# Performance work log

Measured on AMD Instinct MI355X. Metric: run time of the kernel, lower is better.

## Reference

```python
import jax, jax.numpy as jnp
import numpy as np

B, T, N, PRED, DM = 16, 512, 128, 256, 32
L = T + PRED  # 768; conv windows 12 then 4: 768 -> 64 -> 16
EPS = 1e-5


def _conv1d(x, w, b, stride):
    # x: [B, C, L'], w: [C, C, k], kernel_size == stride, VALID (matches torch Conv1d)
    out = jax.lax.conv_general_dilated(x, w, (stride,), 'VALID',
                                       dimension_numbers=('NCH', 'OIH', 'NCH'))
    return out + b[None, :, None]


def _conv2d(x, w, b, pad):
    out = jax.lax.conv_general_dilated(x, w, (1, 1), [(pad, pad), (pad, pad)],
                                       dimension_numbers=('NCHW', 'OIHW', 'NCHW'))
    return out + b[None, :, None, None]


def _bn1d(x, g, b):
    # BatchNorm1d, training-mode batch statistics over (batch, length) per channel
    mu = x.mean((0, 2), keepdims=True)
    var = ((x - mu) ** 2).mean((0, 2), keepdims=True)
    return (x - mu) * jax.lax.rsqrt(var + EPS) * g[None, :, None] + b[None, :, None]


def _cubic_spline(y, size):
    # Natural cubic spline through values y: [B, Lk, C] at knots t = linspace(0,1,Lk),
    # evaluated at linspace(0,1,size). Natural BC: second derivative M=0 at endpoints.
    Bb, Lk, C = y.shape
    h = 1.0 / (Lk - 1)
    # tridiagonal system for interior second derivatives (uniform knots):
    # M[i-1] + 4 M[i] + M[i+1] = 6 * (y[i+1] - 2 y[i] + y[i-1]) / h^2
    m = Lk - 2
    rhs = (y[:, 2:, :] - 2.0 * y[:, 1:-1, :] + y[:, :-2, :]) * (6.0 / (h * h))  # [B,m,C]
    A = 4.0 * jnp.eye(m, dtype=y.dtype) + jnp.eye(m, k=1, dtype=y.dtype) + jnp.eye(m, k=-1, dtype=y.dtype)
    Mi = jnp.linalg.solve(A, rhs.transpose(1, 0, 2).reshape(m, Bb * C))  # [m, B*C]
    Mi = Mi.reshape(m, Bb, C).transpose(1, 0, 2)
    M = jnp.pad(Mi, ((0, 0), (1, 1), (0, 0)))  # [B, Lk, C], M[0]=M[-1]=0
    q = jnp.linspace(0.0, 1.0, size).astype(y.dtype)
    idx = jnp.clip(jnp.floor(q * (Lk - 1)).astype(jnp.int32), 0, Lk - 2)  # [size]
    s = (q - idx.astype(y.dtype) * h)[None, :, None]  # offset within interval
    u = h - s
    yi, yi1 = y[:, idx, :], y[:, idx + 1, :]
    M0, M1 = M[:, idx, :], M[:, idx + 1, :]
    hh6 = h * h / 6.0
    return ((M0 * u ** 3 + M1 * s ** 3) / (6.0 * h)
            + (yi - M0 * hh6) * (u / h)
            + (yi1 - M1 * hh6) * (s / h))  # [B, size, C]


def _forward(batch_x, le_w, le_b, c1_w, c1_b, bn1_g, bn1_b, c2_w, c2_b, bn2_g, bn2_b,
             i1_w0, i1_b0, i1_w1, i1_b1, i2_w0, i2_b0, i2_w1, i2_b1, ld_w, ld_b):
    # instance norm over time
    means = batch_x.mean(1, keepdims=True)
    xc = batch_x - means
    stdev = jnp.sqrt(xc.var(axis=1, keepdims=True) + EPS)
    xn = xc / stdev                               # [B, T, N]
    x = xn.transpose(0, 2, 1)                     # [B, N, T]
    x = jnp.einsum('bnt,lt->bnl', x, le_w) + le_b  # length_encoder -> [B, N, L]
    # multi-scale downsampling conv + spline back up to L
    scales = []
    t = x
    for win, cw, cb, g, bb in ((12, c1_w, c1_b, bn1_g, bn1_b), (4, c2_w, c2_b, bn2_g, bn2_b)):
        t = jax.nn.elu(_bn1d(_conv1d(t, cw, cb, win), g, bb))      # [B, N, L//...]
        scales.append(_cubic_spline(t.transpose(0, 2, 1), L).transpose(0, 2, 1))  # [B, N, L]
    a = jnp.stack([x] + scales, axis=1).transpose(0, 1, 3, 2)  # [B, 3, L, N]
    # Inception block 1 (num_kernels=2: 1x1 and 3x3, averaged), Dropout(eval)=id, GELU(exact)
    h1 = 0.5 * (_conv2d(a, i1_w0, i1_b0, 0) + _conv2d(a, i1_w1, i1_b1, 1))  # [B, DM, L, N]
    h1 = jax.nn.gelu(h1, approximate=False)
    # Inception block 2 -> 1 channel
    h2 = 0.5 * (_conv2d(h1, i2_w0, i2_b0, 0) + _conv2d(h1, i2_w1, i2_b1, 1))  # [B, 1, L, N]
    co = x + h2[:, 0].transpose(0, 2, 1)          # residual, [B, N, L]
    f = jnp.einsum('bnl,pl->bnp', co, ld_w) + ld_b  # length_decoder -> [B, N, PRED]
    f = f.transpose(0, 2, 1)                      # [B, PRED, N]
    return f * stdev[:, 0, :][:, None, :] + means[:, 0, :][:, None, :]


def setup_inputs():
    key = jax.random.key(0)
    ks = jax.random.split(key, 20)
    def w(i, shape, scale=0.02):
        return scale * jax.random.normal(ks[i], shape, jnp.float32)
    return dict(
        batch_x=jax.random.normal(ks[0], (B, T, N), jnp.float32),
        batch_x_mark=jax.random.normal(ks[1], (B, T, 4), jnp.float32),
        dec_inp=jax.random.normal(ks[2], (B, PRED, N), jnp.float32),
        batch_y_mark=jax.random.normal(ks[3], (B, PRED, 4), jnp.float32),
        le_w=w(4, (L, T)), le_b=w(5, (L,)),
        c1_w=w(6, (N, N, 12)), c1_b=w(7, (N,)),
        bn1_g=jnp.ones((N,), jnp.float32), bn1_b=jnp.zeros((N,), jnp.float32),
        c2_w=w(8, (N, N, 4)), c2_b=w(9, (N,)),
        bn2_g=jnp.ones((N,), jnp.float32), bn2_b=jnp.zeros((N,), jnp.float32),
        i1_w0=w(10, (DM, 3, 1, 1), 0.1), i1_b0=jnp.zeros((DM,), jnp.float32),
        i1_w1=w(11, (DM, 3, 3, 3), 0.1), i1_b1=jnp.zeros((DM,), jnp.float32),
        i2_w0=w(12, (1, DM, 1, 1), 0.1), i2_b0=jnp.zeros((1,), jnp.float32),
        i2_w1=w(13, (1, DM, 3, 3), 0.1), i2_b1=jnp.zeros((1,), jnp.float32),
        ld_w=w(14, (PRED, L)), ld_b=w(15, (PRED,)),
    )


def reference(batch_x, batch_x_mark, dec_inp, batch_y_mark, le_w, le_b,
              c1_w, c1_b, bn1_g, bn1_b, c2_w, c2_b, bn2_g, bn2_b,
              i1_w0, i1_b0, i1_w1, i1_b1, i2_w0, i2_b0, i2_w1, i2_b1, ld_w, ld_b):
    # batch_x_mark / dec_inp / batch_y_mark are accepted but unused (as in the torch forward)
    return _forward(batch_x, le_w, le_b, c1_w, c1_b, bn1_g, bn1_b, c2_w, c2_b, bn2_g, bn2_b,
                    i1_w0, i1_b0, i1_w1, i1_b1, i2_w0, i2_b0, i2_w1, i2_b1, ld_w, ld_b)
```

## Files before the change

kernel.cpp:

```cpp
#include <hip/hip_runtime.h>
#include <hip/hip_bf16.h>
#include <math.h>

#define BB 16
#define TT 512
#define NN 128
#define PREDN 256
#define DMC 32
#define LL 768
constexpr float EPSF = 1e-5f;
using bf16 = __hip_bfloat16;
using frag_ab = __attribute__((ext_vector_type(8))) short;
using frag_cd = __attribute__((ext_vector_type(4))) float;

__device__ __forceinline__ unsigned pbf2(float a, float b){
  union { bf16 h; unsigned short u; } x, y;
  x.h = __float2bfloat16(a); y.h = __float2bfloat16(b);
  return (unsigned)x.u | ((unsigned)y.u << 16);
}

__device__ __forceinline__ unsigned short bf16b(float v){
  union { bf16 h; unsigned short u; } x;
  x.h = __float2bfloat16(v);
  return x.u;
}

__device__ __forceinline__ float gelu_fast(float s){
  float s2v = s*s;
  float e = exp2f(s*fmaf(s2v, 0.10294396f, 2.30211806f));
  return s*e*__builtin_amdgcn_rcpf(e + 1.f);
}

__global__ void k_pre(const float* __restrict__ bx, const float* __restrict__ v0,
                      const float* __restrict__ v1, const float* __restrict__ w1c,
                      const float* __restrict__ w2c, const float* __restrict__ w0s1,
                      const float* __restrict__ w1s1, const float* __restrict__ b0s1,
                      const float* __restrict__ b1s1, const float* __restrict__ lew,
                      const float* __restrict__ ldw,
                      float* __restrict__ muv, float* __restrict__ sdv,
                      unsigned short* __restrict__ xbf,
                      float* __restrict__ wT1, float* __restrict__ wT2,
                      uint4* __restrict__ bwpk, uint4* __restrict__ awpk,
                      float* __restrict__ bsum, unsigned* __restrict__ lewbf,
                      unsigned* __restrict__ ldwbf){
  __shared__ float sr[32][16], s2r[32][16], bmu[16], brs[16];
  __shared__ float ts[32][33];
  int blk = blockIdx.x;
  int tid = threadIdx.x;
  if(blk < 128){
    int b = blk >> 3, n0 = (blk & 7)*16;
    int c4 = (tid & 3)*4;
    int ch = tid >> 2;
    const float* p = bx + ((size_t)b*TT + ch*16)*NN + n0 + c4;
    float4 s = make_float4(0.f,0.f,0.f,0.f), s2 = make_float4(0.f,0.f,0.f,0.f);
    for(int t=0;t<16;t++){
      float4 v = *(const float4*)(p + (size_t)t*NN);
      s.x += v.x; s.y += v.y; s.z += v.z; s.w += v.w;
      s2.x += v.x*v.x; s2.y += v.y*v.y; s2.z += v.z*v.z; s2.w += v.w*v.w;
    }
    *(float4*)&sr[ch][c4] = s;
    *(float4*)&s2r[ch][c4] = s2;
    __syncthreads();
    if(tid < 16){
      float ss = 0.f, ss2 = 0.f;
      #pragma unroll 8
      for(int k2=0;k2<32;k2++){ ss += sr[k2][tid]; ss2 += s2r[k2][tid]; }
      float m = ss*(1.f/512.f);
      float var = fmaxf(ss2*(1.f/512.f) - m*m, 0.f);
      float sd = sqrtf(var + EPSF);
      muv[b*NN + n0 + tid] = m;
      sdv[b*NN + n0 + tid] = sd;
      bmu[tid] = m; brs[tid] = 1.f/sd;
    }
    __syncthreads();
    for(int i=tid; i<2048; i+=128){
      int t = i >> 2, g4 = (i & 3)*4;
      const float* q = bx + ((size_t)b*TT + t)*NN + n0 + g4;
      float4 v = *(const float4*)q;
      unsigned lo = pbf2((v.x - bmu[g4  ])*brs[g4  ], (v.y - bmu[g4+1])*brs[g4+1]);
      unsigned hi = pbf2((v.z - bmu[g4+2])*brs[g4+2], (v.w - bmu[g4+3])*brs[g4+3]);
      *(uint2*)&xbf[((size_t)b*TT + t)*NN + n0 + g4] = make_uint2(lo, hi);
    }
  } else if(blk < 320){
    int tt = blk - 128;
    int kt = tt % 48, ot = tt / 48;
    int k0 = kt*32, o0 = ot*32;
    for(int i=tid;i<1024;i+=128){ int r=i>>5, c=i&31; ts[r][c] = w1c[(size_t)(o0+r)*1536 + k0+c]; }
    __syncthreads();
    for(int i=tid;i<1024;i+=128){ int kr=i>>5, oc=i&31; wT1[(size_t)(k0+kr)*NN + o0+oc] = ts[oc][kr]; }
  } else if(blk < 384){
    int tt = blk - 320;
    int kt = tt % 16, ot = tt / 16;
    int k0 = kt*32, o0 = ot*32;
    for(int i=tid;i<1024;i+=128){ int r=i>>5, c=i&31; ts[r][c] = w2c[(size_t)(o0+r)*512 + k0+c]; }
    __syncthreads();
    for(int i=tid;i<1024;i+=128){ int kr=i>>5, oc=i&31; wT2[(size_t)(k0+kr)*NN + o0+oc] = ts[oc][kr]; }
  } else if(blk == 384){
    int i = tid;
    {
      int c = i >> 2, kq = i & 3;
      float w8[8];
      #pragma unroll
      for(int j=0;j<8;j++){
        int k = kq*8+j; float w = 0.f;
        if(k < 27){
          int ci = k/9, r9 = k - ci*9, dy = r9/3, dx = r9 - dy*3;
          w = 0.5f*w1s1[((c*3+ci)*3+dy)*3+dx];
          if(dy==1 && dx==1) w += 0.5f*w0s1[c*3+ci];
        }
        w8[j] = w;
      }
      bwpk[i] = make_uint4(pbf2(w8[0],w8[1]), pbf2(w8[2],w8[3]),
                           pbf2(w8[4],w8[5]), pbf2(w8[6],w8[7]));
    }
    if(i < 36){
      int tap = i >> 2, qq = i & 3, c8 = qq*8;
      float w8[8];
      #pragma unroll
      for(int j=0;j<8;j++){
        int c = c8 + j;
        w8[j] = 0.5f*v1[c*9 + tap] + ((tap==4) ? 0.5f*v0[c] : 0.f);
      }
      awpk[i] = make_uint4(pbf2(w8[0],w8[1]), pbf2(w8[2],w8[3]),
                           pbf2(w8[4],w8[5]), pbf2(w8[6],w8[7]));
    }
    if(i < 32) bsum[i] = 0.5f*(b0s1[i] + b1s1[i]);
  } else if(blk < 513){
    int o = blk - 385;
    for(int i=tid; i<1536; i+=128){
      int l = o*6 + i/256, tp = i%256;
      lewbf[(size_t)l*256 + tp] = pbf2(lew[(size_t)l*TT + 2*tp], lew[(size_t)l*TT + 2*tp + 1]);
    }
  } else {
    int o = blk - 513;
    for(int i=tid; i<1536; i+=128){
      int p = o*4 + i/384, tp = i%384;
      ldwbf[(size_t)p*384 + tp] = pbf2(ldw[(size_t)p*LL + 2*tp], ldw[(size_t)p*LL + 2*tp + 1]);
    }
  }
}

__global__ __launch_bounds__(256) void k_gemm1(const unsigned short* __restrict__ xbf,
    const unsigned* __restrict__ lewbf, const float* __restrict__ leb,
    float* __restrict__ x, float* __restrict__ a0){
  __shared__ unsigned Asu[64*20];
  __shared__ unsigned Bsu[64*20];
  int tid = threadIdx.x;
  int row0 = blockIdx.x*64, l0 = blockIdx.y*64;
  int b = row0 >> 7, n0 = row0 & 127;
  int lane = tid & 63, wv = tid >> 6;
  frag_cd acc[4] = {};
  int an = tid & 63, akq = (tid >> 6)*8;
  int btk = tid & 15, blc = tid >> 4;
  unsigned ra[4], rbq[4];
  #pragma unroll
  for(int u=0;u<4;u++){
    unsigned lo = xbf[((size_t)b*TT + akq + 2*u)*NN + n0 + an];
    unsigned hi = xbf[((size_t)b*TT + akq + 2*u + 1)*NN + n0 + an];
    ra[u] = lo | (hi << 16);
    rbq[u] = lewbf[(size_t)(l0 + blc + 16*u)*256 + btk];
  }
  int fr = wv*16 + (lane & 15);
  int fq = (lane >> 4)*4;
  for(int k0=0;k0<TT;k0+=32){
    *(uint4*)&Asu[an*20 + (akq>>1)] = make_uint4(ra[0], ra[1], ra[2], ra[3]);
    #pragma unroll
    for(int p=0;p<4;p++) Bsu[(blc + 16*p)*20 + btk] = rbq[p];
    __syncthreads();
    if(k0 + 32 < TT){
      #pragma unroll
      for(int u=0;u<4;u++){
        unsigned lo = xbf[((size_t)b*TT + k0 + 32 + akq + 2*u)*NN + n0 + an];
        unsigned hi = xbf[((size_t)b*TT + k0 + 32 + akq + 2*u + 1)*NN + n0 + an];
        ra[u] = lo | (hi << 16);
        rbq[u] = lewbf[(size_t)(l0 + blc + 16*u)*256 + ((k0 + 32) >> 1) + btk];
      }
    }
    frag_ab af = *(const frag_ab*)&Asu[fr*20 + fq];
    #pragma unroll
    for(int nt=0;nt<4;nt++){
      frag_ab bf = *(const frag_ab*)&Bsu[(nt*16 + (lane & 15))*20 + fq];
      acc[nt] = __builtin_amdgcn_mfma_f32_16x16x32_bf16(af, bf, acc[nt], 0, 0, 0);
    }
    __syncthreads();
  }
  int col = lane & 15, quad = lane >> 4;
  #pragma unroll
  for(int nt=0;nt<4;nt++){
    int l = l0 + nt*16 + col;
    float lb = leb[l];
    #pragma unroll
    for(int r=0;r<4;r++){
      int m = wv*16 + quad*4 + r;
      x[(size_t)(row0 + m)*LL + l] = acc[nt][r] + lb;
    }
    float4 st;
    st.x = acc[nt][0] + lb;
    st.y = acc[nt][1] + lb;
    st.z = acc[nt][2] + lb;
    st.w = acc[nt][3] + lb;
    *(float4*)&a0[((size_t)b*LL + l)*NN + n0 + wv*16 + quad*4] = st;
  }
}

__global__ __launch_bounds__(512) void k_conv1(const float* __restrict__ x, const float* __restrict__ wT,
                                               const float* __restrict__ bias, float* __restrict__ t1){
  __shared__ alignas(16) float xs[NN*48];
  int jt = blockIdx.x, b = blockIdx.y;
  int tid = threadIdx.x;
  int o = tid & 127, jj = tid >> 7;
  for(int i=tid;i<NN*48;i+=512){
    int ci = i/48, kk = i%48;
    xs[i] = x[((size_t)b*NN + ci)*LL + jt*48 + kk];
  }
  __syncthreads();
  float a0 = 0.f, a1 = 0.f, a2 = 0.f, a3 = 0.f;
  for(int ci=0;ci<NN;ci++){
    const float* xc = xs + ci*48 + jj*12;
    const float* wc = wT + (size_t)(ci*12)*NN + o;
    #pragma unroll
    for(int kk=0;kk<12;kk+=4){
      a0 = fmaf(xc[kk+0], wc[(size_t)(kk+0)*NN], a0);
      a1 = fmaf(xc[kk+1], wc[(size_t)(kk+1)*NN], a1);
      a2 = fmaf(xc[kk+2], wc[(size_t)(kk+2)*NN], a2);
      a3 = fmaf(xc[kk+3], wc[(size_t)(kk+3)*NN], a3);
    }
  }
  int j = jt*4 + jj;
  t1[((size_t)b*NN + o)*64 + j] = (a0 + a1) + (a2 + a3) + bias[o];
}

__global__ void k_bnstats(const float* __restrict__ t, const float* __restrict__ g, const float* __restrict__ bb,
                          int Bcnt, int Jcnt, float* __restrict__ scale, float* __restrict__ shift){
  int o = blockIdx.x;
  int tot = Bcnt*Jcnt;
  float s = 0.f, s2 = 0.f;
  for(int i=threadIdx.x; i<tot; i+=blockDim.x){
    int b = i / Jcnt, j = i % Jcnt;
    float v = t[((size_t)b*NN + o)*Jcnt + j];
    s += v; s2 += v*v;
  }
  __shared__ float rs[256], rs2[256];
  rs[threadIdx.x] = s; rs2[threadIdx.x] = s2;
  __syncthreads();
  for(int st=128; st>0; st>>=1){
    if(threadIdx.x < st){ rs[threadIdx.x] += rs[threadIdx.x+st]; rs2[threadIdx.x] += rs2[threadIdx.x+st]; }
    __syncthreads();
  }
  if(threadIdx.x == 0){
    float mu = rs[0]/tot;
    float var = fmaxf(rs2[0]/tot - mu*mu, 0.f);
    float sc = g[o] * rsqrtf(var + EPSF);
    scale[o] = sc; shift[o] = bb[o] - mu*sc;
  }
}

template<int LK>
__global__ __launch_bounds__(256) void k_bnspl(const float* __restrict__ t, const float* __restrict__ scale,
    const float* __restrict__ shift, float* __restrict__ tt, float* __restrict__ M){
  constexpr int m = LK-2;
  __shared__ float yt[LK][NN+1];
  __shared__ float cp[m];
  __shared__ float dp[m][NN];
  int b = blockIdx.x, tid = threadIdx.x;
  for(int i=tid; i<LK*NN; i+=256){
    int o = i / LK, j = i - o*LK;
    float v = t[((size_t)b*NN + o)*LK + j]*scale[o] + shift[o];
    v = v > 0.f ? v : (expf(v) - 1.f);
    yt[j][o] = v;
  }
  if(tid == 0){
    float cv = 0.25f; cp[0] = cv;
    for(int i=1;i<m;i++){ cv = 1.f/(4.f - cv); cp[i] = cv; }
  }
  __syncthreads();
  for(int i=tid; i<LK*NN; i+=256){
    int j = i >> 7, o = i & 127;
    tt[((size_t)b*LK + j)*NN + o] = yt[j][o];
  }
  if(tid < NN){
    int c = tid;
    const float Kc = 6.f*(LK-1)*(LK-1);
    float y0 = yt[0][c], y1 = yt[1][c];
    float dprev = 0.f;
    for(int i=0;i<m;i++){
      float y2 = yt[i+2][c];
      float r = (y2 - 2.f*y1 + y0)*Kc;
      float d = (i == 0) ? r*0.25f : (r - dprev)*cp[i];
      dp[i][c] = d; dprev = d;
      y0 = y1; y1 = y2;
    }
    float* Mb = M + (size_t)b*LK*NN + c;
    float xv = dp[m-1][c];
    Mb[(size_t)m*NN] = xv;
    for(int i=m-2;i>=0;i--){
      xv = dp[i][c] - cp[i]*xv;
      Mb[(size_t)(i+1)*NN] = xv;
    }
    Mb[0] = 0.f;
    Mb[(size_t)(LK-1)*NN] = 0.f;
  }
}

__global__ __launch_bounds__(512) void k_conv2(const float* __restrict__ tt, const float* __restrict__ wT,
                                               const float* __restrict__ bias, float* __restrict__ t2){
  __shared__ alignas(16) float ts[16*NN];
  int jt = blockIdx.x, b = blockIdx.y;
  int tid = threadIdx.x;
  int o = tid & 127, jj = tid >> 7;
  for(int i=tid;i<16*NN;i+=512)
    ts[i] = tt[((size_t)b*64 + jt*16)*NN + i];
  __syncthreads();
  float a0 = 0.f, a1 = 0.f, a2 = 0.f, a3 = 0.f;
  for(int ci=0;ci<NN;ci++){
    const float* wc = wT + (size_t)(ci*4)*NN + o;
    const float* tc2 = ts + (jj*4)*NN + ci;
    a0 = fmaf(tc2[0*NN], wc[0*NN], a0);
    a1 = fmaf(tc2[1*NN], wc[1*NN], a1);
    a2 = fmaf(tc2[2*NN], wc[2*NN], a2);
    a3 = fmaf(tc2[3*NN], wc[3*NN], a3);
  }
  int j = jt*4 + jj;
  t2[((size_t)b*NN + o)*16 + j] = (a0 + a1) + (a2 + a3) + bias[o];
}

template<int LK>
__device__ __forceinline__ void spline_pair(const float* __restrict__ y, const float* __restrict__ M,
    int l, int b, int c0, bool ok0, bool ok1, float& v0, float& v1){
  const float hh = 1.f/(LK-1);
  float q = (float)l * (1.f/(LL-1));
  int idx = (int)floorf(q*(LK-1));
  if(idx > LK-2) idx = LK-2;
  float s = q - idx*hh;
  float u = hh - s;
  const float hh6 = hh*hh/6.f;
  const float i6h = 1.f/(6.f*hh);
  const float ih = 1.f/hh;
  float cu = u*u*u, cs = s*s*s;
  float uh = u*ih, sh = s*ih;
  const float* yb = y + ((size_t)b*LK + idx)*NN + c0;
  const float* Mb = M + ((size_t)b*LK + idx)*NN + c0;
  v0 = 0.f; v1 = 0.f;
  if(ok0){
    float yi = yb[0], yi1 = yb[NN], M0 = Mb[0], M1 = Mb[NN];
    v0 = (M0*cu + M1*cs)*i6h + (yi - M0*hh6)*uh + (yi1 - M1*hh6)*sh;
  }
  if(ok1){
    float yi = yb[1], yi1 = yb[NN+1], M0 = Mb[1], M1 = Mb[NN+1];
    v1 = (M0*cu + M1*cs)*i6h + (yi - M0*hh6)*uh + (yi1 - M1*hh6)*sh;
  }
}

#define PBQ 1416
__global__ __launch_bounds__(256, 5) void k_h12(const float* __restrict__ a0,
    const float* __restrict__ y64, const float* __restrict__ M64,
    const float* __restrict__ y16, const float* __restrict__ M16,
    const uint4* __restrict__ bwpk, const uint4* __restrict__ awpk,
    const float* __restrict__ bsum, const float* __restrict__ vb0,
    const float* __restrict__ vb1, unsigned short* __restrict__ cobf){
  __shared__ alignas(16) unsigned short AsBf[3*12*36];
  __shared__ alignas(16) unsigned Au[4*PBQ];
  int tid = threadIdx.x;
  int l0 = blockIdx.x*8, n0 = blockIdx.y*32, b = blockIdx.z;
  int lane = tid & 63, wv = tid >> 6;
  int colB = lane & 15, qg = lane >> 4;

  for(int i=tid; i<648; i+=256){
    int ch = i/216, rem = i%216, yy = rem/18, xxp = rem%18;
    int xx = xxp*2;
    int gl = l0 + yy - 2, gn0 = n0 + xx - 2;
    bool okl = (gl >= 0 && gl < LL);
    bool ok0 = okl && ((unsigned)gn0 < (unsigned)NN);
    bool ok1 = okl && ((unsigned)(gn0+1) < (unsigned)NN);
    float v0 = 0.f, v1 = 0.f;
    if(ch == 0){
      if(ok0) v0 = a0[((size_t)b*LL + gl)*NN + gn0];
      if(ok1) v1 = a0[((size_t)b*LL + gl)*NN + gn0 + 1];
    } else if(okl){
      if(ch == 1) spline_pair<64>(y64, M64, gl, b, gn0, ok0, ok1, v0, v1);
      else        spline_pair<16>(y16, M16, gl, b, gn0, ok0, ok1, v0, v1);
    }
    *(unsigned*)&AsBf[i*2] = pbf2(v0, v1);
  }

  union U4 { uint4 q; frag_ab f; };
  U4 bw0, bw1;
  bw0.q = bwpk[colB*4 + qg];
  bw1.q = bwpk[(colB + 16)*4 + qg];
  float brA[4], brB[4];
  #pragma unroll
  for(int r=0;r<4;r++){ brA[r] = bsum[qg*4 + r]; brB[r] = bsum[16 + qg*4 + r]; }
  __syncthreads();

  {
    const unsigned* Uv = (const unsigned*)AsBf;
    if(tid < 176){
      if(tid < 170){
        int yy = tid/17, xp = tid - yy*17;
        unsigned g[3][3][2];
        #pragma unroll
        for(int ci=0;ci<3;ci++)
          #pragma unroll
          for(int dy=0;dy<3;dy++){
            int base = (ci*12 + yy + dy)*18 + xp;
            g[ci][dy][0] = Uv[base];
            g[ci][dy][1] = Uv[base+1];
          }
        int px0 = yy*34 + 2*xp;
        uint4 pq;
        pq.x = g[0][0][0];
        pq.y = (g[0][0][1]&0xffffu) | (g[0][1][0]<<16);
        pq.z = (g[0][1][0]>>16) | (g[0][1][1]<<16);
        pq.w = g[0][2][0];
        *(uint4*)&Au[0*PBQ + px0*4] = pq;
        pq.x = (g[0][2][1]&0xffffu) | (g[1][0][0]<<16);
        pq.y = (g[1][0][0]>>16) | (g[1][0][1]<<16);
        pq.z = g[1][1][0];
        pq.w = (g[1][1][1]&0xffffu) | (g[1][2][0]<<16);
        *(uint4*)&Au[1*PBQ + px0*4] = pq;
        pq.x = (g[1][2][0]>>16) | (g[1][2][1]<<16);
        pq.y = g[2][0][0];
        pq.z = (g[2][0][1]&0xffffu) | (g[2][1][0]<<16);
        pq.w = (g[2][1][0]>>16) | (g[2][1][1]<<16);
        *(uint4*)&Au[2*PBQ + px0*4] = pq;
        pq.x = g[2][2][0];
        pq.y = g[2][2][1]&0xffffu;
        pq.z = 0u; pq.w = 0u;
        *(uint4*)&Au[3*PBQ + px0*4] = pq;
        int px1 = px0 + 1;
        pq.x = (g[0][0][0]>>16) | (g[0][0][1]<<16);
        pq.y = (g[0][0][1]>>16) | (g[0][1][0]&0xffff0000u);
        pq.z = g[0][1][1];
        pq.w = (g[0][2][0]>>16) | (g[0][2][1]<<16);
        *(uint4*)&Au[0*PBQ + px1*4] = pq;
        pq.x = (g[0][2][1]>>16) | (g[1][0][0]&0xffff0000u);
        pq.y = g[1][0][1];
        pq.z = (g[1][1][0]>>16) | (g[1][1][1]<<16);
        pq.w = (g[1][1][1]>>16) | (g[1][2][0]&0xffff0000u);
        *(uint4*)&Au[1*PBQ + px1*4] = pq;
        pq.x = g[1][2][1];
        pq.y = (g[2][0][0]>>16) | (g[2][0][1]<<16);
        pq.z = (g[2][0][1]>>16) | (g[2][1][0]&0xffff0000u);
        pq.w = g[2][1][1];
        *(uint4*)&Au[2*PBQ + px1*4] = pq;
        pq.x = (g[2][2][0]>>16) | (g[2][2][1]<<16);
        pq.y = g[2][2][1]>>16;
        pq.z = 0u; pq.w = 0u;
        *(uint4*)&Au[3*PBQ + px1*4] = pq;
      } else {
        int px = 340 + (tid-170)*2;
        uint4 z = make_uint4(0u,0u,0u,0u);
        #pragma unroll
        for(int q=0;q<4;q++){
          *(uint4*)&Au[q*PBQ + px*4]     = z;
          *(uint4*)&Au[q*PBQ + (px+1)*4] = z;
        }
      }
    }
  }
  __syncthreads();

  unsigned short* h1h = (unsigned short*)Au;
  frag_cd zac = {0.f, 0.f, 0.f, 0.f};
  for(int t = wv; t < 22; t += 4){
    int px = t*16 + colB;
    U4 av;
    av.q = *(const uint4*)&Au[qg*PBQ + px*4];
    frag_cd d0 = __builtin_amdgcn_mfma_f32_16x16x32_bf16(bw0.f, av.f, zac, 0, 0, 0);
    frag_cd d1 = __builtin_amdgcn_mfma_f32_16x16x32_bf16(bw1.f, av.f, zac, 0, 0, 0);
    unsigned u0 = pbf2(gelu_fast(d0[0] + brA[0]), gelu_fast(d0[1] + brA[1]));
    unsigned u1 = pbf2(gelu_fast(d0[2] + brA[2]), gelu_fast(d0[3] + brA[3]));
    unsigned u2 = pbf2(gelu_fast(d1[0] + brB[0]), gelu_fast(d1[1] + brB[1]));
    unsigned u3 = pbf2(gelu_fast(d1[2] + brB[2]), gelu_fast(d1[3] + brB[3]));
    int lo = (qg >> 1)*PBQ + px*4 + (qg & 1)*2;
    *(uint2*)&Au[lo]           = make_uint2(u0, u1);
    *(uint2*)&Au[2*PBQ + lo]   = make_uint2(u2, u3);
  }
  __syncthreads();

  if(n0 == 0){
    for(int i=tid;i<10*32;i+=256){ int yy=i>>5, ch=i&31;
      h1h[((ch>>3)*PBQ + (yy*34)*4)*2 + (ch&7)] = 0; }
  }
  if(n0 == 96){
    for(int i=tid;i<10*32;i+=256){ int yy=i>>5, ch=i&31;
      h1h[((ch>>3)*PBQ + (yy*34+33)*4)*2 + (ch&7)] = 0; }
  }
  if(l0 == 0){
    for(int i=tid;i<34*32;i+=256){ int xx=i>>5, ch=i&31;
      h1h[((ch>>3)*PBQ + xx*4)*2 + (ch&7)] = 0; }
  }
  if(l0 == 760){
    for(int i=tid;i<34*32;i+=256){ int xx=i>>5, ch=i&31;
      h1h[((ch>>3)*PBQ + (9*34+xx)*4)*2 + (ch&7)] = 0; }
  }

  U4 aw[9];
  #pragma unroll
  for(int tap=0; tap<9; tap++) aw[tap].q = awpk[tap*4 + qg];
  float vbsum = vb0[0] + vb1[0];
  __syncthreads();

  frag_cd cacc[4] = {};
  int baseoff[4];
  #pragma unroll
  for(int tt=0; tt<4; tt++){
    int px = (wv*4 + tt)*16 + colB;
    int yy = px >> 5, xx = px & 31;
    baseoff[tt] = qg*PBQ + (yy*34 + xx)*4;
  }
  #pragma unroll
  for(int dy=0; dy<3; dy++)
    #pragma unroll
    for(int dx=0; dx<3; dx++){
      int tap = dy*3 + dx;
      int off = (dy*34 + dx)*4;
      #pragma unroll
      for(int tt=0; tt<4; tt++){
        U4 bv;
        bv.q = *(const uint4*)&Au[baseoff[tt] + off];
        cacc[tt] = __builtin_amdgcn_mfma_f32_16x16x32_bf16(aw[tap].f, bv.f, cacc[tt], 0, 0, 0);
      }
    }
  if(lane < 16){
    #pragma unroll
    for(int tt=0; tt<4; tt++){
      int px = (wv*4 + tt)*16 + lane;
      int yy = px >> 5, xx = px & 31;
      size_t idx = ((size_t)b*LL + l0 + yy)*NN + n0 + xx;
      cobf[idx] = bf16b(cacc[tt][0] + vbsum + a0[idx]);
    }
  }
}

__global__ __launch_bounds__(256) void k_gemm2(const unsigned short* __restrict__ cobf,
    const unsigned* __restrict__ ldwbf, const float* __restrict__ ldb,
    const float* __restrict__ muv, const float* __restrict__ sdv,
    float* __restrict__ out){
  __shared__ unsigned Asu[64*20];
  __shared__ unsigned Bsu[32*20];
  int tid = threadIdx.x;
  int row0 = blockIdx.x*64, p0 = blockIdx.y*32;
  int b = row0 >> 7, n0 = row0 & 127;
  int lane = tid & 63, wv = tid >> 6;
  frag_cd acc[2] = {};
  int an = tid & 63, akq = (tid >> 6)*8;
  int btk = tid & 15, blc = tid >> 4;
  unsigned ra[4], rbq[2];
  #pragma unroll
  for(int u=0;u<4;u++){
    unsigned lo = cobf[((size_t)b*LL + akq + 2*u)*NN + n0 + an];
    unsigned hi = cobf[((size_t)b*LL + akq + 2*u + 1)*NN + n0 + an];
    ra[u] = lo | (hi << 16);
  }
  #pragma unroll
  for(int u=0;u<2;u++)
    rbq[u] = ldwbf[(size_t)(p0 + blc + 16*u)*384 + btk];
  int fr = wv*16 + (lane & 15);
  int fq = (lane >> 4)*4;
  for(int k0=0;k0<LL;k0+=32){
    *(uint4*)&Asu[an*20 + (akq>>1)] = make_uint4(ra[0], ra[1], ra[2], ra[3]);
    #pragma unroll
    for(int p=0;p<2;p++) Bsu[(blc + 16*p)*20 + btk] = rbq[p];
    __syncthreads();
    if(k0 + 32 < LL){
      #pragma unroll
      for(int u=0;u<4;u++){
        unsigned lo = cobf[((size_t)b*LL + k0 + 32 + akq + 2*u)*NN + n0 + an];
        unsigned hi = cobf[((size_t)b*LL + k0 + 32 + akq + 2*u + 1)*NN + n0 + an];
        ra[u] = lo | (hi << 16);
      }
      #pragma unroll
      for(int u=0;u<2;u++)
        rbq[u] = ldwbf[(size_t)(p0 + blc + 16*u)*384 + ((k0 + 32) >> 1) + btk];
    }
    frag_ab af = *(const frag_ab*)&Asu[fr*20 + fq];
    #pragma unroll
    for(int nt=0;nt<2;nt++){
      frag_ab bf = *(const frag_ab*)&Bsu[(nt*16 + (lane & 15))*20 + fq];
      acc[nt] = __builtin_amdgcn_mfma_f32_16x16x32_bf16(af, bf, acc[nt], 0, 0, 0);
    }
    __syncthreads();
  }
  int col = lane & 15, quad = lane >> 4;
  float mu_r[4], sd_r[4];
  #pragma unroll
  for(int r=0;r<4;r++){
    int row = row0 + wv*16 + quad*4 + r;
    mu_r[r] = muv[row];
    sd_r[r] = sdv[row];
  }
  #pragma unroll
  for(int nt=0;nt<2;nt++){
    int p = p0 + nt*16 + col;
    float lb = ldb[p];
    float4 st;
    st.x = (acc[nt][0] + lb)*sd_r[0] + mu_r[0];
    st.y = (acc[nt][1] + lb)*sd_r[1] + mu_r[1];
    st.z = (acc[nt][2] + lb)*sd_r[2] + mu_r[2];
    st.w = (acc[nt][3] + lb)*sd_r[3] + mu_r[3];
    *(float4*)&out[((size_t)b*PREDN + p)*NN + n0 + wv*16 + quad*4] = st;
  }
}

extern "C" void kernel_launch(void* const* d_in, const int* in_sizes, int n_in,
                              void* d_out, int out_size, void* d_ws, size_t ws_size,
                              hipStream_t stream){
  (void)in_sizes; (void)n_in; (void)out_size; (void)ws_size;
  const float* batch_x = (const float*)d_in[0];
  const float* le_w  = (const float*)d_in[4];
  const float* le_b  = (const float*)d_in[5];
  const float* c1_w  = (const float*)d_in[6];
  const float* c1_b  = (const float*)d_in[7];
  const float* bn1_g = (const float*)d_in[8];
  const float* bn1_b = (const float*)d_in[9];
  const float* c2_w  = (const float*)d_in[10];
  const float* c2_b  = (const float*)d_in[11];
  const float* bn2_g = (const float*)d_in[12];
  const float* bn2_b = (const float*)d_in[13];
  const float* i1_w0 = (const float*)d_in[14];
  const float* i1_b0 = (const float*)d_in[15];
  const float* i1_w1 = (const float*)d_in[16];
  const float* i1_b1 = (const float*)d_in[17];
  const float* i2_w0 = (const float*)d_in[18];
  const float* i2_b0 = (const float*)d_in[19];
  const float* i2_w1 = (const float*)d_in[20];
  const float* i2_b1 = (const float*)d_in[21];
  const float* ld_w  = (const float*)d_in[22];
  const float* ld_b  = (const float*)d_in[23];
  float* out = (float*)d_out;

  float* ws   = (float*)d_ws;
  float* muv  = ws;
  float* sdv  = muv + 2048;
  float* wT1  = sdv + 2048;
  float* wT2  = wT1 + 196608;
  float* x    = wT2 + 65536;
  float* a0   = x + (size_t)BB*NN*LL;
  float* t1   = a0 + (size_t)BB*LL*NN;
  float* t1t  = t1 + (size_t)BB*NN*64;
  float* Msp1 = t1t + (size_t)BB*64*NN;
  float* t2   = Msp1 + (size_t)BB*64*NN;
  float* t2t  = t2 + (size_t)BB*NN*16;
  float* Msp2 = t2t + (size_t)BB*16*NN;
  float* sc1  = Msp2 + (size_t)BB*16*NN;
  float* sh1  = sc1 + NN;
  float* sc2  = sh1 + NN;
  float* sh2  = sc2 + NN;
  float* fB1  = sh2 + NN;
  unsigned short* xbf = (unsigned short*)fB1;
  float* fB2  = fB1 + 524288;
  unsigned* lewbf = (unsigned*)fB2;
  float* fB3  = fB2 + 196608;
  unsigned* ldwbf = (unsigned*)fB3;
  float* fB4  = fB3 + 98304;
  uint4* bwpk = (uint4*)fB4;
  float* fB5  = fB4 + 512;
  uint4* awpk = (uint4*)fB5;
  float* fB6  = fB5 + 144;
  float* bsum = fB6;
  float* fB7  = fB6 + 32;
  unsigned short* cobf = (unsigned short*)fB7;

  k_pre<<<577, 128, 0, stream>>>(batch_x, i2_w0, i2_w1, c1_w, c2_w,
                                 i1_w0, i1_w1, i1_b0, i1_b1, le_w, ld_w,
                                 muv, sdv, xbf, wT1, wT2, bwpk, awpk, bsum, lewbf, ldwbf);
  k_gemm1<<<dim3(32,12), 256, 0, stream>>>(xbf, lewbf, le_b, x, a0);
  k_conv1<<<dim3(16,BB), 512, 0, stream>>>(x, wT1, c1_b, t1);
  k_bnstats<<<NN, 256, 0, stream>>>(t1, bn1_g, bn1_b, BB, 64, sc1, sh1);
  k_bnspl<64><<<BB, 256, 0, stream>>>(t1, sc1, sh1, t1t, Msp1);
  k_conv2<<<dim3(4,BB), 512, 0, stream>>>(t1t, wT2, c2_b, t2);
  k_bnstats<<<NN, 256, 0, stream>>>(t2, bn2_g, bn2_b, BB, 16, sc2, sh2);
  k_bnspl<16><<<BB, 256, 0, stream>>>(t2, sc2, sh2, t2t, Msp2);
  k_h12<<<dim3(96,4,BB), 256, 0, stream>>>(a0, t1t, Msp1, t2t, Msp2,
                                           bwpk, awpk, bsum, i2_b0, i2_b1, cobf);
  k_gemm2<<<dim3(32,8), 256, 0, stream>>>(cobf, ldwbf, ld_b, muv, sdv, out);
}
```

Before: 257.5 us.

## Split conv1 over input-channel groups and drop redundant x output from gemm1

gemm1 no longer writes the channel-major copy x; conv1 reads the transposed a0 buffer directly and is split four ways over input channels, raising the grid from 256 to 1024 blocks. Each split writes a partial-sum slab, and the BN stats and BN+spline kernels sum the four partials plus the conv bias on load. This removes one full-size store from gemm1 and improves conv1 occupancy. In exchange it writes and rereads partial buffers four times larger, and the shared-memory load in conv1 is a transposing gather.

Measured after the change: 258.7 us. Within noise of the previous version (+0.4%).

```diff
diff --git a/kernel.cpp b/kernel.cpp
--- a/kernel.cpp
+++ b/kernel.cpp
@@ -142,7 +142,7 @@
 
 __global__ __launch_bounds__(256) void k_gemm1(const unsigned short* __restrict__ xbf,
     const unsigned* __restrict__ lewbf, const float* __restrict__ leb,
-    float* __restrict__ x, float* __restrict__ a0){
+    float* __restrict__ a0){
   __shared__ unsigned Asu[64*20];
   __shared__ unsigned Bsu[64*20];
   int tid = threadIdx.x;
@@ -189,11 +189,6 @@
   for(int nt=0;nt<4;nt++){
     int l = l0 + nt*16 + col;
     float lb = leb[l];
-    #pragma unroll
-    for(int r=0;r<4;r++){
-      int m = wv*16 + quad*4 + r;
-      x[(size_t)(row0 + m)*LL + l] = acc[nt][r] + lb;
-    }
     float4 st;
     st.x = acc[nt][0] + lb;
     st.y = acc[nt][1] + lb;
@@ -203,31 +198,66 @@
   }
 }
 
-__global__ __launch_bounds__(512) void k_conv1(const float* __restrict__ x, const float* __restrict__ wT,
-                                               const float* __restrict__ bias, float* __restrict__ t1){
-  __shared__ alignas(16) float xs[NN*48];
-  int jt = blockIdx.x, b = blockIdx.y;
+__global__ __launch_bounds__(512) void k_conv1(const float* __restrict__ a0v, const float* __restrict__ wT,
+                                               float* __restrict__ t1p){
+  __shared__ alignas(16) float xs[32][52];
+  int jt = blockIdx.x, b = blockIdx.y, ks = blockIdx.z;
   int tid = threadIdx.x;
   int o = tid & 127, jj = tid >> 7;
-  for(int i=tid;i<NN*48;i+=512){
-    int ci = i/48, kk = i%48;
-    xs[i] = x[((size_t)b*NN + ci)*LL + jt*48 + kk];
+  for(int i=tid;i<1536;i+=512){
+    int lp = i >> 5, np = i & 31;
+    xs[np][lp] = a0v[((size_t)b*LL + jt*48 + lp)*NN + ks*32 + np];
   }
   __syncthreads();
   float a0 = 0.f, a1 = 0.f, a2 = 0.f, a3 = 0.f;
-  for(int ci=0;ci<NN;ci++){
-    const float* xc = xs + ci*48 + jj*12;
+  for(int cp=0;cp<32;cp++){
+    int ci = ks*32 + cp;
+    const float4* xc = (const float4*)(&xs[cp][jj*12]);
+    float4 xv0 = xc[0], xv1 = xc[1], xv2 = xc[2];
     const float* wc = wT + (size_t)(ci*12)*NN + o;
-    #pragma unroll
-    for(int kk=0;kk<12;kk+=4){
-      a0 = fmaf(xc[kk+0], wc[(size_t)(kk+0)*NN], a0);
-      a1 = fmaf(xc[kk+1], wc[(size_t)(kk+1)*NN], a1);
-      a2 = fmaf(xc[kk+2], wc[(size_t)(kk+2)*NN], a2);
-      a3 = fmaf(xc[kk+3], wc[(size_t)(kk+3)*NN], a3);
-    }
+    a0 = fmaf(xv0.x, wc[(size_t)0*NN],  a0);
+    a1 = fmaf(xv0.y, wc[(size_t)1*NN],  a1);
+    a2 = fmaf(xv0.z, wc[(size_t)2*NN],  a2);
+    a3 = fmaf(xv0.w, wc[(size_t)3*NN],  a3);
+    a0 = fmaf(xv1.x, wc[(size_t)4*NN],  a0);
+    a1 = fmaf(xv1.y, wc[(size_t)5*NN],  a1);
+    a2 = fmaf(xv1.z, wc[(size_t)6*NN],  a2);
+    a3 = fmaf(xv1.w, wc[(size_t)7*NN],  a3);
+    a0 = fmaf(xv2.x, wc[(size_t)8*NN],  a0);
+    a1 = fmaf(xv2.y, wc[(size_t)9*NN],  a1);
+    a2 = fmaf(xv2.z, wc[(size_t)10*NN], a2);
+    a3 = fmaf(xv2.w, wc[(size_t)11*NN], a3);
   }
   int j = jt*4 + jj;
-  t1[((size_t)b*NN + o)*64 + j] = (a0 + a1) + (a2 + a3) + bias[o];
+  t1p[(((size_t)ks*BB + b)*NN + o)*64 + j] = (a0 + a1) + (a2 + a3);
+}
+
+#define T1PS ((size_t)BB*NN*64)
+
+__global__ void k_bnstats4(const float* __restrict__ t1p, const float* __restrict__ cb,
+                           const float* __restrict__ g, const float* __restrict__ bb,
+                           float* __restrict__ scale, float* __restrict__ shift){
+  int o = blockIdx.x;
+  float s = 0.f, s2 = 0.f;
+  for(int i=threadIdx.x; i<1024; i+=256){
+    int b = i >> 6, j = i & 63;
+    size_t base = ((size_t)b*NN + o)*64 + j;
+    float v = t1p[base] + t1p[T1PS + base] + t1p[2*T1PS + base] + t1p[3*T1PS + base] + cb[o];
+    s += v; s2 += v*v;
+  }
+  __shared__ float rs[256], rs2[256];
+  rs[threadIdx.x] = s; rs2[threadIdx.x] = s2;
+  __syncthreads();
+  for(int st=128; st>0; st>>=1){
+    if(threadIdx.x < st){ rs[threadIdx.x] += rs[threadIdx.x+st]; rs2[threadIdx.x] += rs2[threadIdx.x+st]; }
+    __syncthreads();
+  }
+  if(threadIdx.x == 0){
+    float mu = rs[0]/1024.f;
+    float var = fmaxf(rs2[0]/1024.f - mu*mu, 0.f);
+    float sc = g[o] * rsqrtf(var + EPSF);
+    scale[o] = sc; shift[o] = bb[o] - mu*sc;
+  }
 }
 
 __global__ void k_bnstats(const float* __restrict__ t, const float* __restrict__ g, const float* __restrict__ bb,
@@ -252,6 +282,55 @@
     float var = fmaxf(rs2[0]/tot - mu*mu, 0.f);
     float sc = g[o] * rsqrtf(var + EPSF);
     scale[o] = sc; shift[o] = bb[o] - mu*sc;
+  }
+}
+
+__global__ __launch_bounds__(256) void k_bnspl64p(const float* __restrict__ t1p, const float* __restrict__ cb,
+    const float* __restrict__ scale, const float* __restrict__ shift,
+    float* __restrict__ tt, float* __restrict__ M){
+  constexpr int LK = 64, m = LK-2;
+  __shared__ float yt[LK][NN+1];
+  __shared__ float cp[m];
+  __shared__ float dp[m][NN];
+  int b = blockIdx.x, tid = threadIdx.x;
+  for(int i=tid; i<LK*NN; i+=256){
+    int o = i / LK, j = i - o*LK;
+    size_t base = ((size_t)b*NN + o)*64 + j;
+    float v = t1p[base] + t1p[T1PS + base] + t1p[2*T1PS + base] + t1p[3*T1PS + base] + cb[o];
+    v = v*scale[o] + shift[o];
+    v = v > 0.f ? v : (expf(v) - 1.f);
+    yt[j][o] = v;
+  }
+  if(tid == 0){
+    float cv = 0.25f; cp[0] = cv;
+    for(int i=1;i<m;i++){ cv = 1.f/(4.f - cv); cp[i] = cv; }
+  }
+  __syncthreads();
+  for(int i=tid; i<LK*NN; i+=256){
+    int j = i >> 7, o = i & 127;
+    tt[((size_t)b*LK + j)*NN + o] = yt[j][o];
+  }
+  if(tid < NN){
+    int c = tid;
+    const float Kc = 6.f*(LK-1)*(LK-1);
+    float y0 = yt[0][c], y1 = yt[1][c];
+    float dprev = 0.f;
+    for(int i=0;i<m;i++){
+      float y2 = yt[i+2][c];
+      float r = (y2 - 2.f*y1 + y0)*Kc;
+      float d = (i == 0) ? r*0.25f : (r - dprev)*cp[i];
+      dp[i][c] = d; dprev = d;
+      y0 = y1; y1 = y2;
+    }
+    float* Mb = M + (size_t)b*LK*NN + c;
+    float xv = dp[m-1][c];
+    Mb[(size_t)m*NN] = xv;
+    for(int i=m-2;i>=0;i--){
+      xv = dp[i][c] - cp[i]*xv;
+      Mb[(size_t)(i+1)*NN] = xv;
+    }
+    Mb[0] = 0.f;
+    Mb[(size_t)(LK-1)*NN] = 0.f;
   }
 }
 
@@ -635,10 +714,9 @@
   float* sdv  = muv + 2048;
   float* wT1  = sdv + 2048;
   float* wT2  = wT1 + 196608;
-  float* x    = wT2 + 65536;
-  float* a0   = x + (size_t)BB*NN*LL;
-  float* t1   = a0 + (size_t)BB*LL*NN;
-  float* t1t  = t1 + (size_t)BB*NN*64;
+  float* a0   = wT2 + 65536;
+  float* t1p  = a0 + (size_t)BB*LL*NN;
+  float* t1t  = t1p + 4*T1PS;
   float* Msp1 = t1t + (size_t)BB*64*NN;
   float* t2   = Msp1 + (size_t)BB*64*NN;
   float* t2t  = t2 + (size_t)BB*NN*16;
@@ -665,10 +743,10 @@
   k_pre<<<577, 128, 0, stream>>>(batch_x, i2_w0, i2_w1, c1_w, c2_w,
                                  i1_w0, i1_w1, i1_b0, i1_b1, le_w, ld_w,
                                  muv, sdv, xbf, wT1, wT2, bwpk, awpk, bsum, lewbf, ldwbf);
-  k_gemm1<<<dim3(32,12), 256, 0, stream>>>(xbf, lewbf, le_b, x, a0);
-  k_conv1<<<dim3(16,BB), 512, 0, stream>>>(x, wT1, c1_b, t1);
-  k_bnstats<<<NN, 256, 0, stream>>>(t1, bn1_g, bn1_b, BB, 64, sc1, sh1);
-  k_bnspl<64><<<BB, 256, 0, stream>>>(t1, sc1, sh1, t1t, Msp1);
+  k_gemm1<<<dim3(32,12), 256, 0, stream>>>(xbf, lewbf, le_b, a0);
+  k_conv1<<<dim3(16,BB,4), 512, 0, stream>>>(a0, wT1, t1p);
+  k_bnstats4<<<NN, 256, 0, stream>>>(t1p, c1_b, bn1_g, bn1_b, sc1, sh1);
+  k_bnspl64p<<<BB, 256, 0, stream>>>(t1p, c1_b, sc1, sh1, t1t, Msp1);
   k_conv2<<<dim3(4,BB), 512, 0, stream>>>(t1t, wT2, c2_b, t2);
   k_bnstats<<<NN, 256, 0, stream>>>(t2, bn2_g, bn2_b, BB, 16, sc2, sh2);
   k_bnspl<16><<<BB, 256, 0, stream>>>(t2, sc2, sh2, t2t, Msp2);
```
